# Performance work log

Hardware: AMD Instinct MI355X
Metric: run time of the kernel (lower is better)

## Reference

```python
import jax, jax.numpy as jnp
import numpy as np

B, CIN, COUT, H, W = 16, 128, 128, 64, 64
E, PS, FF = 8, 16, 8
GC, HID, HC = 4 * FF, 64, COUT * 4  # gate_channel, gate hidden, bottleneck hidden


def conv(x, w, stride=1, pad=0, groups=1):
    # x: [B,C,H,W], w: [O,I/groups,kh,kw]
    return jax.lax.conv_general_dilated(
        x, w, (stride, stride), [(pad, pad), (pad, pad)], feature_group_count=groups)


def group_norm(x, scale, bias, groups, eps=1e-5):
    b, c = x.shape[:2]
    xr = x.reshape(b, groups, c // groups, *x.shape[2:])
    m = xr.mean(axis=(2, 3, 4), keepdims=True)
    v = xr.var(axis=(2, 3, 4), keepdims=True)
    xr = (xr - m) * jax.lax.rsqrt(v + eps)
    return xr.reshape(x.shape) * scale[None, :, None, None] + bias[None, :, None, None]


def setup_inputs() -> dict:
    key = jax.random.key(0)
    ks = jax.random.split(key, 8)
    f = lambda k, shp: jax.random.normal(k, shp, jnp.float32) * 0.05
    return dict(
        x=jax.random.normal(ks[0], (B, CIN, H, W), jnp.float32),
        w_exp=f(ks[1], (E, COUT, CIN, 3, 3)),
        gn_exp_s=jnp.ones((E, COUT), jnp.float32),
        gn_exp_b=jnp.zeros((E, COUT), jnp.float32),
        w1=f(ks[2], (GC, HID)), b1=jnp.zeros((HID,), jnp.float32),
        w2=f(ks[3], (HID, E)), b2=jnp.zeros((E,), jnp.float32),
        w_pw1=f(ks[4], (HC, COUT, 1, 1)),
        gn1_s=jnp.ones((HC,), jnp.float32), gn1_b=jnp.zeros((HC,), jnp.float32),
        w_dw=f(ks[5], (HC, 1, 3, 3)),
        gn2_s=jnp.ones((HC,), jnp.float32), gn2_b=jnp.zeros((HC,), jnp.float32),
        w_pw2=f(ks[6], (COUT, HC, 1, 1)),
        gn3_s=jnp.ones((COUT,), jnp.float32), gn3_b=jnp.zeros((COUT,), jnp.float32),
    )


def reference(x, w_exp, gn_exp_s, gn_exp_b, w1, b1, w2, b2,
              w_pw1, gn1_s, gn1_b, w_dw, gn2_s, gn2_b, w_pw2, gn3_s, gn3_b):
    # ---- Conv experts (residual 3x3 conv + GN + SiLU), vmapped over experts ----
    def expert(w, s, b):
        y = conv(x, w, pad=1)
        y = group_norm(y, s, b, groups=min(8, COUT))
        return jax.nn.silu(y) + x  # use_residual=True, CIN == COUT

    ys = jax.vmap(expert)(w_exp, gn_exp_s, gn_exp_b)  # [E,B,C,H,W]

    # ---- Router gate: Fourier features of patch-center coordinates ----
    ph, pw = H // PS, W // PS
    cy = (jnp.arange(ph, dtype=jnp.float32) + 0.5) / ph
    cx = (jnp.arange(pw, dtype=jnp.float32) + 0.5) / pw
    freqs = (2.0 ** jnp.arange(FF, dtype=jnp.float32)) * jnp.pi
    ay = cy[:, None] * freqs  # [ph,FF]
    ax = cx[:, None] * freqs  # [pw,FF]
    feats = jnp.concatenate([
        jnp.broadcast_to(jnp.sin(ay)[:, None, :], (ph, pw, FF)),
        jnp.broadcast_to(jnp.cos(ay)[:, None, :], (ph, pw, FF)),
        jnp.broadcast_to(jnp.sin(ax)[None, :, :], (ph, pw, FF)),
        jnp.broadcast_to(jnp.cos(ax)[None, :, :], (ph, pw, FF)),
    ], axis=-1)  # [ph,pw,4*FF] == gate_channel
    hgate = jax.nn.silu(feats @ w1 + b1)
    wts = jax.nn.softmax(hgate @ w2 + b2, axis=-1)  # [ph,pw,E]

    # ---- Patch-wise combine of expert outputs ----
    wmap = jnp.repeat(jnp.repeat(wts, PS, axis=0), PS, axis=1)  # [H,W,E]
    combined = jnp.einsum('ebchw,hwe->bchw', ys, wmap)

    # ---- Inverted bottleneck: 1x1 -> dw3x3 -> 1x1(stride2) with GN+SiLU ----
    h = jax.nn.silu(group_norm(conv(combined, w_pw1), gn1_s, gn1_b, groups=8))
    h = jax.nn.silu(group_norm(conv(h, w_dw, pad=1, groups=HC), gn2_s, gn2_b, groups=8))
    h = jax.nn.silu(group_norm(conv(h, w_pw2, stride=2), gn3_s, gn3_b, groups=8))
    return h  # [B, COUT, H//2, W//2]
```

## Files before the change

kernel.cpp:

```cpp
#include <hip/hip_runtime.h>
#include <hip/hip_bf16.h>


#define B_ 16
#define CIN_ 128
#define COUT_ 128
#define H_ 64
#define W_ 64
#define HW_ 4096
#define E_ 8
#define FF_ 8
#define GC_ 32
#define HID_ 64
#define HC_ 512

typedef __hip_bfloat16 bf16;
typedef __bf16 bf16x8 __attribute__((ext_vector_type(8)));
typedef float f32x4 __attribute__((ext_vector_type(4)));
typedef float f32x16 __attribute__((ext_vector_type(16)));

__device__ __forceinline__ float siluf(float v) {
  return v * __builtin_amdgcn_rcpf(1.f + __expf(-v));
}
__device__ __forceinline__ float bf2f(bf16 v) { return __bfloat162float(v); }
__device__ __forceinline__ bf16 f2bf(float v) { return __float2bfloat16(v); }

__device__ __forceinline__ void async16(void* lds, const void* g) {
  __builtin_amdgcn_global_load_lds(
      (const __attribute__((address_space(1))) unsigned int*)g,
      (__attribute__((address_space(3))) unsigned int*)lds, 16, 0, 0);
}

__global__ void gate_kernel(const float* __restrict__ w1, const float* __restrict__ b1,
                            const float* __restrict__ w2, const float* __restrict__ b2,
                            float* __restrict__ wts) {
  int p = threadIdx.x;
  if (p >= 16) return;
  int i = p >> 2, j = p & 3;
  float cy = (i + 0.5f) * 0.25f;
  float cx = (j + 0.5f) * 0.25f;
  float feats[GC_];
#pragma unroll
  for (int f = 0; f < FF_; ++f) {
    float fr = 3.14159265358979f * (float)(1 << f);
    float ay = cy * fr, ax = cx * fr;
    feats[f] = sinf(ay);
    feats[FF_ + f] = cosf(ay);
    feats[2 * FF_ + f] = sinf(ax);
    feats[3 * FF_ + f] = cosf(ax);
  }
  float hid[HID_];
  for (int k = 0; k < HID_; ++k) {
    float a = b1[k];
#pragma unroll
    for (int m = 0; m < GC_; ++m) a = fmaf(feats[m], w1[m * HID_ + k], a);
    hid[k] = siluf(a);
  }
  float lg[E_];
  float mx = -1e30f;
#pragma unroll
  for (int e = 0; e < E_; ++e) {
    float a = b2[e];
    for (int k = 0; k < HID_; ++k) a = fmaf(hid[k], w2[k * E_ + e], a);
    lg[e] = a;
    mx = fmaxf(mx, a);
  }
  float s = 0.f;
#pragma unroll
  for (int e = 0; e < E_; ++e) { lg[e] = __expf(lg[e] - mx); s += lg[e]; }
  float inv = 1.f / s;
#pragma unroll
  for (int e = 0; e < E_; ++e) wts[p * E_ + e] = lg[e] * inv;
}

__global__ __launch_bounds__(256) void xt_kernel(const float* __restrict__ x,
                                                 bf16* __restrict__ xT) {
  __shared__ float t[128][65];
  int b = blockIdx.x >> 6, h = blockIdx.x & 63;
  int tid = threadIdx.x;
  int w = tid & 63, c4 = tid >> 6;
  const float* xb = x + ((size_t)(b * 128) * 64 + h) * 64;
#pragma unroll 4
  for (int rep = 0; rep < 32; ++rep) {
    int ci = rep * 4 + c4;
    t[ci][w] = xb[(size_t)ci * HW_ + w];
  }
  __syncthreads();
  bf16* dst = xT + (size_t)(b * 64 + h) * 8192;
#pragma unroll 4
  for (int rep = 0; rep < 32; ++rep) {
    int o = rep * 256 + tid;
    int cg = o >> 9, w2 = (o >> 3) & 63, lo = o & 7;
    dst[o] = f2bf(t[cg * 8 + lo][w2]);
  }
}

__global__ void wt_kernel(const float* __restrict__ w_exp, bf16* __restrict__ wT) {
  int idx = blockIdx.x * 256 + threadIdx.x;
  if (idx >= 1179648) return;
  int lo = idx & 7;
  int co = (idx >> 3) & 127;
  int cg = (idx >> 10) & 15;
  int rest = idx >> 14;
  int tap = rest % 9, e = rest / 9;
  int ci = cg * 8 + lo;
  wT[idx] = f2bf(w_exp[(((size_t)(e * 128 + co) * 128 + ci) * 9) + tap]);
}

__global__ void wpT_kernel(const float* __restrict__ w_pw1, const float* __restrict__ w_pw2,
                           bf16* __restrict__ wp1T, bf16* __restrict__ wp2T) {
  int idx = blockIdx.x * 256 + threadIdx.x;
  if (idx < 65536) wp1T[idx] = f2bf(w_pw1[idx]);
  else if (idx < 131072) wp2T[idx - 65536] = f2bf(w_pw2[idx - 65536]);
}

__global__ __launch_bounds__(256, 2) void conv_mfma(
    const bf16* __restrict__ xT, const bf16* __restrict__ wT,
    float* __restrict__ statsE, bf16* __restrict__ ys) {
  __shared__ __align__(16) char xls[4 * 6336];
  __shared__ __align__(16) char wls[2][3 * 8192];
  __shared__ float red[4][8][2];

  int blk = blockIdx.x;
  int xcd = blk & 7;
  int r2 = blk >> 3;
  int b = xcd * 2 + (r2 & 1);
  int rest = r2 >> 1;
  int rt = rest & 15, e = rest >> 4;

  int tid = threadIdx.x, lane = tid & 63, wave = tid >> 6;
  int hi = lane >> 5, l31 = lane & 31;
  int h0 = rt * 4;

  if (tid < 48) {
    int cg = tid / 12, rem = tid % 12;
    int r = rem >> 1, edge = rem & 1;
    *(uint4*)(xls + cg * 6336 + r * 1056 + edge * 1040) = make_uint4(0u, 0u, 0u, 0u);
  }
  int rbad = (rt == 0) ? 0 : (rt == 15 ? 5 : -1);
  if (rbad >= 0) {
    int cg = tid >> 6, slot = (tid & 63) + 1;
    *(uint4*)(xls + cg * 6336 + rbad * 1056 + slot * 16) = make_uint4(0u, 0u, 0u, 0u);
  }

  f32x16 acc[4][2];
#pragma unroll
  for (int mt = 0; mt < 4; ++mt)
#pragma unroll
    for (int nt = 0; nt < 2; ++nt)
#pragma unroll
      for (int r = 0; r < 16; ++r) acc[mt][nt][r] = 0.f;

  for (int q = 0; q < 4; ++q) {
    if (q) __syncthreads();
    {
      int cg = wave;
#pragma unroll
      for (int r = 0; r < 6; ++r) {
        int h = h0 - 1 + r;
        if ((unsigned)h < 64u) {
          const char* g = (const char*)xT +
              ((size_t)((b * 64 + h) * 16) + q * 4 + cg) * 1024 + lane * 16;
          async16(xls + cg * 6336 + r * 1056 + 16, g);
        }
      }
    }
#pragma unroll
    for (int s = 0; s < 6; ++s) {
      int seg = wave * 6 + s;
      int tap = seg >> 3, rem = seg & 7;
      int cg = rem >> 1, cb = rem & 1;
      const char* g = (const char*)wT +
          ((size_t)(((e * 9 + tap) * 16) + q * 4 + cg) * 128 + cb * 64) * 16 + lane * 16;
      async16(wls[0] + (tap * 4 + cg) * 2048 + cb * 1024, g);
    }
    __syncthreads();

    for (int dr = 0; dr < 3; ++dr) {
      int buf = dr & 1;
      if (dr < 2) {
#pragma unroll
        for (int s = 0; s < 6; ++s) {
          int seg = wave * 6 + s;
          int tap = seg >> 3, rem = seg & 7;
          int cg = rem >> 1, cb = rem & 1;
          const char* g = (const char*)wT +
              ((size_t)(((e * 9 + (dr + 1) * 3 + tap) * 16) + q * 4 + cg) * 128 + cb * 64) * 16 +
              lane * 16;
          async16(wls[buf ^ 1] + (tap * 4 + cg) * 2048 + cb * 1024, g);
        }
      }
      int r_local = wave + dr;
      const char* wb = wls[buf];
      const char* xrow = xls;
      bf16x8 afp[2][2], bfp[2][2];
      {
        int cgl = hi;
        afp[0][0] = *(const bf16x8*)(wb + cgl * 2048 + (0 * 32 + l31) * 16);
        afp[0][1] = *(const bf16x8*)(wb + cgl * 2048 + (1 * 32 + l31) * 16);
        const char* xr = xrow + cgl * 6336 + r_local * 1056;
        bfp[0][0] = *(const bf16x8*)(xr + (0 * 32 + l31 + 0) * 16);
        bfp[0][1] = *(const bf16x8*)(xr + (1 * 32 + l31 + 0) * 16);
      }
#pragma unroll
      for (int s = 0; s < 12; ++s) {
        int mh = s & 1;
        int cura = s & 1, curb = (s >> 1) & 1;
        if (s < 11) {
          int s1 = s + 1;
          int ds1 = s1 >> 2, ks1 = (s1 >> 1) & 1, mh1 = s1 & 1;
          int cgl1 = ks1 * 2 + hi;
          const char* wt1 = wb + ds1 * 8192 + cgl1 * 2048;
          afp[s1 & 1][0] = *(const bf16x8*)(wt1 + ((mh1 * 2 + 0) * 32 + l31) * 16);
          afp[s1 & 1][1] = *(const bf16x8*)(wt1 + ((mh1 * 2 + 1) * 32 + l31) * 16);
          if (mh1 == 0) {
            const char* xr1 = xrow + cgl1 * 6336 + r_local * 1056;
            bfp[(s1 >> 1) & 1][0] = *(const bf16x8*)(xr1 + (0 * 32 + l31 + ds1) * 16);
            bfp[(s1 >> 1) & 1][1] = *(const bf16x8*)(xr1 + (1 * 32 + l31 + ds1) * 16);
          }
        }
#pragma unroll
        for (int i = 0; i < 2; ++i)
#pragma unroll
          for (int nt = 0; nt < 2; ++nt)
            acc[mh * 2 + i][nt] = __builtin_amdgcn_mfma_f32_32x32x16_bf16(
                afp[cura][i], bfp[curb][nt], acc[mh * 2 + i][nt], 0, 0, 0);
      }
      if (dr < 2) __syncthreads();
    }
  }

  int hh = h0 + wave;
  bf16* yb = ys + (size_t)((e * 16 + b) * 128) * 4096;
#pragma unroll
  for (int mt = 0; mt < 4; ++mt) {
    float s0 = 0.f, ss0 = 0.f, s1 = 0.f, ss1 = 0.f;
#pragma unroll
    for (int nt = 0; nt < 2; ++nt) {
      int w = nt * 32 + l31;
      int pos = hh * 64 + w;
#pragma unroll
      for (int r = 0; r < 16; ++r) {
        float v = acc[mt][nt][r];
        if (r < 8) { s0 += v; ss0 += v * v; } else { s1 += v; ss1 += v * v; }
        int row = (r & 3) + 8 * (r >> 2) + 4 * hi;
        yb[(size_t)(mt * 32 + row) * 4096 + pos] = f2bf(v);
      }
    }
#pragma unroll
    for (int off = 32; off; off >>= 1) {
      s0 += __shfl_down(s0, off, 64);
      ss0 += __shfl_down(ss0, off, 64);
      s1 += __shfl_down(s1, off, 64);
      ss1 += __shfl_down(ss1, off, 64);
    }
    if (lane == 0) {
      red[wave][mt * 2][0] = s0; red[wave][mt * 2][1] = ss0;
      red[wave][mt * 2 + 1][0] = s1; red[wave][mt * 2 + 1][1] = ss1;
    }
  }
  __syncthreads();
  if (tid < 16) {
    int g = tid >> 1, which = tid & 1;
    float t = red[0][g][which] + red[1][g][which] + red[2][g][which] + red[3][g][which];
    atomicAdd(&statsE[((e * 16 + b) * 8 + g) * 2 + which], t);
  }
}

__global__ __launch_bounds__(256) void combine_cl(
    const float* __restrict__ x, const bf16* __restrict__ ys,
    const float* __restrict__ stE, const float* __restrict__ gns,
    const float* __restrict__ gnb, const float* __restrict__ wts,
    bf16* __restrict__ ccl) {
  __shared__ bf16 tile[64][132];
  int b = blockIdx.x >> 6, h = blockIdx.x & 63;
  int t = threadIdx.x;
  int oct = t & 7, cq = t >> 3;
  int w0 = oct * 8;
  int gidx = cq >> 2;
  int pid = (h >> 4) * 4 + (w0 >> 4);
  int pos = h * 64 + w0;

  float m_[8], r_[8], wt_[8];
#pragma unroll
  for (int e = 0; e < 8; ++e) {
    float S = stE[((e * 16 + b) * 8 + gidx) * 2];
    float SS = stE[((e * 16 + b) * 8 + gidx) * 2 + 1];
    float mean = S * (1.f / 65536.f);
    float var = SS * (1.f / 65536.f) - mean * mean;
    m_[e] = mean;
    r_[e] = rsqrtf(var + 1e-5f);
    wt_[e] = wts[pid * 8 + e];
  }

#pragma unroll
  for (int k = 0; k < 4; ++k) {
    int co = cq * 4 + k;
    const float* xp = x + ((size_t)(b * 128 + co) << 12) + pos;
    float v[8];
    float4 xa = *(const float4*)xp;
    float4 xb2 = *(const float4*)(xp + 4);
    v[0] = xa.x; v[1] = xa.y; v[2] = xa.z; v[3] = xa.w;
    v[4] = xb2.x; v[5] = xb2.y; v[6] = xb2.z; v[7] = xb2.w;
#pragma unroll
    for (int e = 0; e < 8; ++e) {
      uint4 u = *(const uint4*)(ys + ((size_t)((e * 16 + b) * 128 + co) << 12) + pos);
      const bf16* pv = (const bf16*)&u;
      float sc = r_[e] * gns[e * 128 + co];
      float sh = gnb[e * 128 + co] - m_[e] * sc;
#pragma unroll
      for (int j = 0; j < 8; ++j) {
        float yn = bf2f(pv[j]) * sc + sh;
        v[j] = fmaf(siluf(yn), wt_[e], v[j]);
      }
    }
#pragma unroll
    for (int j = 0; j < 8; ++j) tile[w0 + j][co] = f2bf(v[j]);
  }
  __syncthreads();
  int row = t >> 2, q = t & 3;
  char* dst = (char*)ccl + ((size_t)(b * 4096 + h * 64 + row)) * 256 + q * 64;
  const char* src = (const char*)&tile[row][0] + q * 64;
#pragma unroll
  for (int i = 0; i < 4; ++i)
    *(uint4*)(dst + i * 16) = *(const uint4*)(src + i * 16);
}

__global__ __launch_bounds__(256) void pw1_mfma(
    const bf16* __restrict__ ccl, const bf16* __restrict__ wp1T,
    bf16* __restrict__ h1cl, float* __restrict__ stats1) {
  __shared__ __align__(16) char ls[65536];
  __shared__ float red[4][2][2];
  char* als = ls;
  char* bls = ls + 32768;
  int blk = blockIdx.x;
  int ntile = blk & 511, mtile = blk >> 9;
  int n0 = ntile * 128, m0 = mtile * 128;
  int t = threadIdx.x, lane = t & 63, wave = t >> 6;
  int quad = lane >> 4, l15 = lane & 15;
  int b = n0 >> 12;

#pragma unroll
  for (int i = 0; i < 8; ++i) {
    int id = t + 256 * i;
    int r = id >> 4, c = id & 15;
    *(uint4*)(als + c * 2048 + r * 16) =
        *(const uint4*)((const char*)wp1T + (size_t)(m0 + r) * 256 + c * 16);
    *(uint4*)(bls + c * 2048 + r * 16) =
        *(const uint4*)((const char*)ccl + (size_t)(n0 + r) * 256 + c * 16);
  }
  __syncthreads();

  f32x4 acc[8][2];
#pragma unroll
  for (int mt = 0; mt < 8; ++mt)
#pragma unroll
    for (int nt = 0; nt < 2; ++nt) acc[mt][nt] = (f32x4){0.f, 0.f, 0.f, 0.f};

#pragma unroll
  for (int kc = 0; kc < 4; ++kc) {
    int cgq = kc * 4 + quad;
    bf16x8 af[8];
#pragma unroll
    for (int mt = 0; mt < 8; ++mt)
      af[mt] = *(const bf16x8*)(als + cgq * 2048 + (mt * 16 + l15) * 16);
    bf16x8 bfr[2];
#pragma unroll
    for (int nt = 0; nt < 2; ++nt)
      bfr[nt] = *(const bf16x8*)(bls + cgq * 2048 + (wave * 32 + nt * 16 + l15) * 16);
#pragma unroll
    for (int mt = 0; mt < 8; ++mt)
#pragma unroll
      for (int nt = 0; nt < 2; ++nt)
        acc[mt][nt] = __builtin_amdgcn_mfma_f32_16x16x32_bf16(
            af[mt], bfr[nt], acc[mt][nt], 0, 0, 0);
  }

  __syncthreads();
  float s[2] = {0.f, 0.f}, ss[2] = {0.f, 0.f};
  bf16* tile = (bf16*)ls;
#pragma unroll
  for (int mt = 0; mt < 8; ++mt) {
    int gi = mt >> 2;
#pragma unroll
    for (int nt = 0; nt < 2; ++nt) {
      int n = wave * 32 + nt * 16 + l15;
#pragma unroll
      for (int r = 0; r < 4; ++r) {
        float v = acc[mt][nt][r];
        s[gi] += v;
        ss[gi] += v * v;
        tile[n * 132 + mt * 16 + quad * 4 + r] = f2bf(v);
      }
    }
  }
#pragma unroll
  for (int gi = 0; gi < 2; ++gi) {
#pragma unroll
    for (int off = 32; off; off >>= 1) {
      s[gi] += __shfl_down(s[gi], off, 64);
      ss[gi] += __shfl_down(ss[gi], off, 64);
    }
  }
  if (lane == 0) {
    red[wave][0][0] = s[0]; red[wave][0][1] = ss[0];
    red[wave][1][0] = s[1]; red[wave][1][1] = ss[1];
  }
  __syncthreads();
  if (t < 4) {
    int gi = t >> 1, which = t & 1;
    float v = red[0][gi][which] + red[1][gi][which] + red[2][gi][which] + red[3][gi][which];
    atomicAdd(&stats1[(b * 8 + mtile * 2 + gi) * 2 + which], v);
  }
#pragma unroll
  for (int i = 0; i < 8; ++i) {
    int id = t + 256 * i;
    int r = id >> 4, q = id & 15;
    char* dst = (char*)h1cl + (size_t)(n0 + r) * 1024 + m0 * 2 + q * 16;
    const char* src = (const char*)tile + r * 264 + q * 16;
    *(uint4*)dst = *(const uint4*)src;
  }
}

__global__ __launch_bounds__(256) void dw_cl(
    const bf16* __restrict__ h1cl, const float* __restrict__ w_dw,
    const float* __restrict__ st1, const float* __restrict__ gs,
    const float* __restrict__ gb, bf16* __restrict__ h2cl,
    float* __restrict__ stats2) {
  __shared__ __align__(16) bf16 tile[18 * 66 * 16];
  __shared__ float red2[4][2];
  int blk = blockIdx.x;
  int ht = blk & 3, hcg = (blk >> 2) & 31, b = blk >> 7;
  int h0 = ht * 16;
  int hc0 = hcg * 16;
  int hcb = hcg >> 2;
  int t = threadIdx.x;

  float S1 = st1[(b * 8 + hcb) * 2], SS1 = st1[(b * 8 + hcb) * 2 + 1];
  float mean = S1 * (1.f / 262144.f);
  float var1 = SS1 * (1.f / 262144.f) - mean * mean;
  float rstd = rsqrtf(var1 + 1e-5f);
  float scale[16], shift[16];
#pragma unroll
  for (int j = 0; j < 16; ++j) {
    float g = gs[hc0 + j];
    scale[j] = rstd * g;
    shift[j] = gb[hc0 + j] - mean * rstd * g;
  }

  for (int i = 0; i < 5; ++i) {
    int idx = t + 256 * i;
    if (idx >= 1188) break;
    int row = idx / 66, wslot = idx - row * 66;
    int hh = h0 - 1 + row;
    int w = wslot - 1;
    int swz = (wslot >> 2) & 3;
    bf16* dst = tile + (row * 66 + wslot) * 16;
    if ((unsigned)hh < 64u && (unsigned)w < 64u) {
      const char* p = (const char*)h1cl + ((size_t)(b * 4096 + hh * 64 + w) * 512 + hc0) * 2;
      uint4 a0 = *(const uint4*)p;
      uint4 a1 = *(const uint4*)(p + 16);
      const bf16* pv = (const bf16*)&a0;
      const bf16* pv1 = (const bf16*)&a1;
      bf16 outv[16];
#pragma unroll
      for (int j = 0; j < 8; ++j)
        outv[j] = f2bf(siluf(bf2f(pv[j]) * scale[j] + shift[j]));
#pragma unroll
      for (int j = 0; j < 8; ++j)
        outv[8 + j] = f2bf(siluf(bf2f(pv1[j]) * scale[8 + j] + shift[8 + j]));
#pragma unroll
      for (int qq = 0; qq < 4; ++qq) {
        int ph = (qq + swz) & 3;
        *(uint2*)(dst + ph * 4) = *(const uint2*)(outv + qq * 4);
      }
    } else {
      *(uint4*)dst = make_uint4(0u, 0u, 0u, 0u);
      *(uint4*)(dst + 8) = make_uint4(0u, 0u, 0u, 0u);
    }
  }
  __syncthreads();

  int w = t & 63, q = t >> 6;
  float wv[9][4];
#pragma unroll
  for (int j = 0; j < 4; ++j) {
    int hc = hc0 + q * 4 + j;
#pragma unroll
    for (int tap = 0; tap < 9; ++tap) wv[tap][j] = w_dw[hc * 9 + tap];
  }

  f32x4 win[3][3];
  float acc_s = 0.f, acc_ss = 0.f;

  auto ld4 = [&](int r, int dwi) -> f32x4 {
    int slot = w + dwi;
    int ph = (q + (slot >> 2)) & 3;
    const bf16* p = tile + (r * 66 + slot) * 16 + ph * 4;
    uint2 u = *(const uint2*)p;
    const bf16* pb = (const bf16*)&u;
    return (f32x4){bf2f(pb[0]), bf2f(pb[1]), bf2f(pb[2]), bf2f(pb[3])};
  };

#pragma unroll
  for (int dwi = 0; dwi < 3; ++dwi) {
    win[0][dwi] = ld4(0, dwi);
    win[1][dwi] = ld4(1, dwi);
  }
#pragma unroll
  for (int orow = 0; orow < 16; ++orow) {
    int rnew = orow + 2;
    int ringn = rnew % 3;
#pragma unroll
    for (int dwi = 0; dwi < 3; ++dwi) win[ringn][dwi] = ld4(rnew, dwi);
    f32x4 acc = (f32x4){0.f, 0.f, 0.f, 0.f};
#pragma unroll
    for (int dr = 0; dr < 3; ++dr) {
      int ring = (orow + dr) % 3;
#pragma unroll
      for (int dwi = 0; dwi < 3; ++dwi) {
#pragma unroll
        for (int j = 0; j < 4; ++j)
          acc[j] = fmaf(win[ring][dwi][j], wv[dr * 3 + dwi][j], acc[j]);
      }
    }
#pragma unroll
    for (int j = 0; j < 4; ++j) { acc_s += acc[j]; acc_ss += acc[j] * acc[j]; }
    if (!(orow & 1) && !(w & 1)) {
      int hglob = h0 + orow;
      int pos2 = (hglob >> 1) * 32 + (w >> 1);
      bf16 tmp[4];
#pragma unroll
      for (int j = 0; j < 4; ++j) tmp[j] = f2bf(acc[j]);
      *(uint2*)((char*)h2cl + ((size_t)(b * 1024 + pos2) * 512 + hc0 + q * 4) * 2) =
          *(const uint2*)tmp;
    }
  }

#pragma unroll
  for (int off = 32; off; off >>= 1) {
    acc_s += __shfl_down(acc_s, off, 64);
    acc_ss += __shfl_down(acc_ss, off, 64);
  }
  int wave = t >> 6;
  if ((t & 63) == 0) { red2[wave][0] = acc_s; red2[wave][1] = acc_ss; }
  __syncthreads();
  if (t < 2) {
    float v = red2[0][t] + red2[1][t] + red2[2][t] + red2[3][t];
    atomicAdd(&stats2[(b * 8 + hcb) * 2 + t], v);
  }
}

__global__ __launch_bounds__(256) void pw2_mfma(
    const bf16* __restrict__ h2, const bf16* __restrict__ wp2T,
    const float* __restrict__ st2, const float* __restrict__ gs2,
    const float* __restrict__ gb2, float* __restrict__ h3,
    float* __restrict__ stats3) {
  __shared__ __align__(16) char als[2][8192];
  __shared__ __align__(16) char bls[2][4096];
  __shared__ float red[4][8][2];
  int blk = blockIdx.x;
  int n0 = blk * 64;
  int b = n0 >> 10, posb = n0 & 1023;
  int t = threadIdx.x, lane = t & 63, wave = t >> 6;
  int quad = lane >> 4, l15 = lane & 15;
  int wbase = wave * 16;
  int c4 = t >> 6, r = t & 63;

  auto load_bls = [&](char* dst, int kc) {
    int hc0 = (kc * 4 + c4) * 8;
    int g = hc0 >> 6;
    float S = st2[(b * 8 + g) * 2], SS = st2[(b * 8 + g) * 2 + 1];
    float mean = S * (1.f / 262144.f);
    float rstd = rsqrtf(SS * (1.f / 262144.f) - mean * mean + 1e-5f);
    uint4 u = *(const uint4*)((const char*)h2 + (size_t)(n0 + r) * 1024 +
                              (size_t)(kc * 4 + c4) * 16);
    const bf16* pv = (const bf16*)&u;
    bf16 outv[8];
#pragma unroll
    for (int j = 0; j < 8; ++j) {
      float xv = bf2f(pv[j]);
      xv = (xv - mean) * rstd * gs2[hc0 + j] + gb2[hc0 + j];
      outv[j] = f2bf(siluf(xv));
    }
    *(uint4*)dst = *(const uint4*)outv;
  };

  f32x4 acc[8];
#pragma unroll
  for (int mt = 0; mt < 8; ++mt) acc[mt] = (f32x4){0.f, 0.f, 0.f, 0.f};

  {
#pragma unroll
    for (int i = 0; i < 2; ++i) {
      int id = t + 256 * i;
      int cc = id >> 7, rr = id & 127;
      *(uint4*)(als[0] + cc * 2048 + rr * 16) =
          *(const uint4*)((const char*)wp2T + (size_t)rr * 1024 + cc * 16);
    }
    load_bls(bls[0] + c4 * 1024 + r * 16, 0);
  }
#pragma unroll
  for (int kc = 0; kc < 16; ++kc) {
    __syncthreads();
    if (kc + 1 < 16) {
      int nb = (kc + 1) & 1;
#pragma unroll
      for (int i = 0; i < 2; ++i) {
        int id = t + 256 * i;
        int cc = id >> 7, rr = id & 127;
        *(uint4*)(als[nb] + cc * 2048 + rr * 16) =
            *(const uint4*)((const char*)wp2T + (size_t)rr * 1024 + ((kc + 1) * 4 + cc) * 16);
      }
      load_bls(bls[nb] + c4 * 1024 + r * 16, kc + 1);
    }
    int buf = kc & 1;
    bf16x8 bf1 = *(const bf16x8*)(bls[buf] + quad * 1024 + (wbase + l15) * 16);
#pragma unroll
    for (int mt = 0; mt < 8; ++mt) {
      bf16x8 af = *(const bf16x8*)(als[buf] + quad * 2048 + (mt * 16 + l15) * 16);
      acc[mt] = __builtin_amdgcn_mfma_f32_16x16x32_bf16(af, bf1, acc[mt], 0, 0, 0);
    }
  }

#pragma unroll
  for (int mt = 0; mt < 8; ++mt) {
    float s = 0.f, ss = 0.f;
    int pos = posb + wbase + l15;
#pragma unroll
    for (int rr = 0; rr < 4; ++rr) {
      float v = acc[mt][rr];
      s += v;
      ss += v * v;
      int co = mt * 16 + quad * 4 + rr;
      h3[(size_t)(b * 128 + co) * 1024 + pos] = v;
    }
#pragma unroll
    for (int off = 32; off; off >>= 1) {
      s += __shfl_down(s, off, 64);
      ss += __shfl_down(ss, off, 64);
    }
    if (lane == 0) { red[wave][mt][0] = s; red[wave][mt][1] = ss; }
  }
  __syncthreads();
  if (t < 16) {
    int mt = t >> 1, which = t & 1;
    float v = red[0][mt][which] + red[1][mt][which] + red[2][mt][which] + red[3][mt][which];
    atomicAdd(&stats3[(b * 8 + mt) * 2 + which], v);
  }
}

__global__ void out_kernel(const float* __restrict__ h3, const float* __restrict__ stats,
                           const float* __restrict__ gs, const float* __restrict__ gb,
                           float* __restrict__ out) {
  const int total = B_ * COUT_ * 1024;
  for (int idx = blockIdx.x * blockDim.x + threadIdx.x; idx < total; idx += gridDim.x * blockDim.x) {
    int c = (idx >> 10) & 127;
    int b = idx >> 17;
    int bg = b * 8 + (c >> 4);
    float S = stats[bg * 2], SS = stats[bg * 2 + 1];
    float mean = S * (1.f / 16384.f);
    float var = SS * (1.f / 16384.f) - mean * mean;
    float rstd = rsqrtf(var + 1e-5f);
    float v = (h3[idx] - mean) * rstd * gs[c] + gb[c];
    out[idx] = siluf(v);
  }
}

extern "C" void kernel_launch(void* const* d_in, const int* in_sizes, int n_in,
                              void* d_out, int out_size, void* d_ws, size_t ws_size,
                              hipStream_t stream) {
  const float* x = (const float*)d_in[0];
  const float* w_exp = (const float*)d_in[1];
  const float* gn_exp_s = (const float*)d_in[2];
  const float* gn_exp_b = (const float*)d_in[3];
  const float* w1 = (const float*)d_in[4];
  const float* b1 = (const float*)d_in[5];
  const float* w2 = (const float*)d_in[6];
  const float* b2 = (const float*)d_in[7];
  const float* w_pw1 = (const float*)d_in[8];
  const float* gn1_s = (const float*)d_in[9];
  const float* gn1_b = (const float*)d_in[10];
  const float* w_dw = (const float*)d_in[11];
  const float* gn2_s = (const float*)d_in[12];
  const float* gn2_b = (const float*)d_in[13];
  const float* w_pw2 = (const float*)d_in[14];
  const float* gn3_s = (const float*)d_in[15];
  const float* gn3_b = (const float*)d_in[16];

  char* ws = (char*)d_ws;
  const size_t WP1T_OFF = 16384;
  const size_t WP2T_OFF = WP1T_OFF + 131072;
  const size_t XT_OFF = WP2T_OFF + 131072;
  const size_t WT_OFF = XT_OFF + 16777216;
  const size_t YS_OFF = WT_OFF + 2359296;
  const size_t NEEDED = YS_OFF + 134217728;
  if (ws_size < NEEDED) return;

  float* wts = (float*)ws;
  float* stats1 = (float*)(ws + 1024);
  float* stats2 = (float*)(ws + 2048);
  float* stats3 = (float*)(ws + 3072);
  float* statsE = (float*)(ws + 4096);
  bf16* wp1T = (bf16*)(ws + WP1T_OFF);
  bf16* wp2T = (bf16*)(ws + WP2T_OFF);
  bf16* xT = (bf16*)(ws + XT_OFF);
  bf16* ccl = (bf16*)(ws + XT_OFF);
  bf16* wT = (bf16*)(ws + WT_OFF);
  bf16* ys = (bf16*)(ws + YS_OFF);
  bf16* h1cl = (bf16*)(ws + YS_OFF);
  bf16* h2cl = (bf16*)(ws + YS_OFF + 67108864);
  float* h3 = (float*)(ws + YS_OFF + 83886080);

  hipMemsetAsync(ws, 0, 16384, stream);
  gate_kernel<<<1, 64, 0, stream>>>(w1, b1, w2, b2, wts);
  xt_kernel<<<B_ * 64, 256, 0, stream>>>(x, xT);
  wt_kernel<<<4608, 256, 0, stream>>>(w_exp, wT);
  wpT_kernel<<<512, 256, 0, stream>>>(w_pw1, w_pw2, wp1T, wp2T);
  conv_mfma<<<E_ * B_ * 16, 256, 0, stream>>>(xT, wT, statsE, ys);
  combine_cl<<<B_ * 64, 256, 0, stream>>>(x, ys, statsE, gn_exp_s, gn_exp_b, wts, ccl);
  pw1_mfma<<<4 * 512, 256, 0, stream>>>(ccl, wp1T, h1cl, stats1);
  dw_cl<<<B_ * 32 * 4, 256, 0, stream>>>(h1cl, w_dw, stats1, gn1_s, gn1_b, h2cl, stats2);
  pw2_mfma<<<256, 256, 0, stream>>>(h2cl, wp2T, stats2, gn2_s, gn2_b, h3, stats3);
  out_kernel<<<1024, 256, 0, stream>>>(h3, stats3, gn3_s, gn3_b, (float*)d_out);
}
```

Baseline: 438.6 us.

## Fuse prep kernels, loop pw1 over M tiles, remap combine blocks, vectorize output

Merges the gate, x-transpose, expert-weight and pointwise-weight conversion kernels into one launch, cutting launch overhead. pw1 now loads each activation tile once and loops over the four output-channel tiles instead of launching a block per tile. combine blocks are remapped so a batch stays on one XCD, presumably to reuse ys in that die's cache. The output GN+SiLU kernel processes float4 per thread with a folded scale/shift. The trade-off is fewer blocks in pw1, which lowers parallelism, plus more serialized work per block.

Result: no change. 437.6 us (-0.2%).

```diff
diff --git a/kernel.cpp b/kernel.cpp
--- a/kernel.cpp
+++ b/kernel.cpp
@@ -31,87 +31,89 @@
       (__attribute__((address_space(3))) unsigned int*)lds, 16, 0, 0);
 }
 
-__global__ void gate_kernel(const float* __restrict__ w1, const float* __restrict__ b1,
-                            const float* __restrict__ w2, const float* __restrict__ b2,
-                            float* __restrict__ wts) {
-  int p = threadIdx.x;
-  if (p >= 16) return;
-  int i = p >> 2, j = p & 3;
-  float cy = (i + 0.5f) * 0.25f;
-  float cx = (j + 0.5f) * 0.25f;
-  float feats[GC_];
-#pragma unroll
-  for (int f = 0; f < FF_; ++f) {
-    float fr = 3.14159265358979f * (float)(1 << f);
-    float ay = cy * fr, ax = cx * fr;
-    feats[f] = sinf(ay);
-    feats[FF_ + f] = cosf(ay);
-    feats[2 * FF_ + f] = sinf(ax);
-    feats[3 * FF_ + f] = cosf(ax);
-  }
-  float hid[HID_];
-  for (int k = 0; k < HID_; ++k) {
-    float a = b1[k];
-#pragma unroll
-    for (int m = 0; m < GC_; ++m) a = fmaf(feats[m], w1[m * HID_ + k], a);
-    hid[k] = siluf(a);
-  }
-  float lg[E_];
-  float mx = -1e30f;
-#pragma unroll
-  for (int e = 0; e < E_; ++e) {
-    float a = b2[e];
-    for (int k = 0; k < HID_; ++k) a = fmaf(hid[k], w2[k * E_ + e], a);
-    lg[e] = a;
-    mx = fmaxf(mx, a);
-  }
-  float s = 0.f;
-#pragma unroll
-  for (int e = 0; e < E_; ++e) { lg[e] = __expf(lg[e] - mx); s += lg[e]; }
-  float inv = 1.f / s;
-#pragma unroll
-  for (int e = 0; e < E_; ++e) wts[p * E_ + e] = lg[e] * inv;
-}
-
-__global__ __launch_bounds__(256) void xt_kernel(const float* __restrict__ x,
-                                                 bf16* __restrict__ xT) {
+__global__ __launch_bounds__(256) void prep_kernel(
+    const float* __restrict__ x, bf16* __restrict__ xT,
+    const float* __restrict__ w_exp, bf16* __restrict__ wT,
+    const float* __restrict__ w_pw1, const float* __restrict__ w_pw2,
+    bf16* __restrict__ wp1T, bf16* __restrict__ wp2T,
+    const float* __restrict__ w1, const float* __restrict__ b1,
+    const float* __restrict__ w2, const float* __restrict__ b2,
+    float* __restrict__ wts) {
   __shared__ float t[128][65];
-  int b = blockIdx.x >> 6, h = blockIdx.x & 63;
+  int blk = blockIdx.x;
   int tid = threadIdx.x;
-  int w = tid & 63, c4 = tid >> 6;
-  const float* xb = x + ((size_t)(b * 128) * 64 + h) * 64;
+
+  if (blk < 1024) {
+    int b = blk >> 6, h = blk & 63;
+    int w = tid & 63, c4 = tid >> 6;
+    const float* xb = x + ((size_t)(b * 128) * 64 + h) * 64;
 #pragma unroll 4
-  for (int rep = 0; rep < 32; ++rep) {
-    int ci = rep * 4 + c4;
-    t[ci][w] = xb[(size_t)ci * HW_ + w];
-  }
-  __syncthreads();
-  bf16* dst = xT + (size_t)(b * 64 + h) * 8192;
+    for (int rep = 0; rep < 32; ++rep) {
+      int ci = rep * 4 + c4;
+      t[ci][w] = xb[(size_t)ci * HW_ + w];
+    }
+    __syncthreads();
+    bf16* dst = xT + (size_t)(b * 64 + h) * 8192;
 #pragma unroll 4
-  for (int rep = 0; rep < 32; ++rep) {
-    int o = rep * 256 + tid;
-    int cg = o >> 9, w2 = (o >> 3) & 63, lo = o & 7;
-    dst[o] = f2bf(t[cg * 8 + lo][w2]);
-  }
-}
-
-__global__ void wt_kernel(const float* __restrict__ w_exp, bf16* __restrict__ wT) {
-  int idx = blockIdx.x * 256 + threadIdx.x;
-  if (idx >= 1179648) return;
-  int lo = idx & 7;
-  int co = (idx >> 3) & 127;
-  int cg = (idx >> 10) & 15;
-  int rest = idx >> 14;
-  int tap = rest % 9, e = rest / 9;
-  int ci = cg * 8 + lo;
-  wT[idx] = f2bf(w_exp[(((size_t)(e * 128 + co) * 128 + ci) * 9) + tap]);
-}
-
-__global__ void wpT_kernel(const float* __restrict__ w_pw1, const float* __restrict__ w_pw2,
-                           bf16* __restrict__ wp1T, bf16* __restrict__ wp2T) {
-  int idx = blockIdx.x * 256 + threadIdx.x;
-  if (idx < 65536) wp1T[idx] = f2bf(w_pw1[idx]);
-  else if (idx < 131072) wp2T[idx - 65536] = f2bf(w_pw2[idx - 65536]);
+    for (int rep = 0; rep < 32; ++rep) {
+      int o = rep * 256 + tid;
+      int cg = o >> 9, w2 = (o >> 3) & 63, lo = o & 7;
+      dst[o] = f2bf(t[cg * 8 + lo][w2]);
+    }
+  } else if (blk < 5632) {
+    int idx = (blk - 1024) * 256 + tid;
+    if (idx < 1179648) {
+      int lo = idx & 7;
+      int co = (idx >> 3) & 127;
+      int cg = (idx >> 10) & 15;
+      int rest = idx >> 14;
+      int tap = rest % 9, e = rest / 9;
+      int ci = cg * 8 + lo;
+      wT[idx] = f2bf(w_exp[(((size_t)(e * 128 + co) * 128 + ci) * 9) + tap]);
+    }
+  } else if (blk < 6144) {
+    int idx = (blk - 5632) * 256 + tid;
+    if (idx < 65536) wp1T[idx] = f2bf(w_pw1[idx]);
+    else wp2T[idx - 65536] = f2bf(w_pw2[idx - 65536]);
+  } else {
+    int p = tid;
+    if (p >= 16) return;
+    int i = p >> 2, j = p & 3;
+    float cy = (i + 0.5f) * 0.25f;
+    float cx = (j + 0.5f) * 0.25f;
+    float feats[GC_];
+#pragma unroll
+    for (int f = 0; f < FF_; ++f) {
+      float fr = 3.14159265358979f * (float)(1 << f);
+      float ay = cy * fr, ax = cx * fr;
+      feats[f] = sinf(ay);
+      feats[FF_ + f] = cosf(ay);
+      feats[2 * FF_ + f] = sinf(ax);
+      feats[3 * FF_ + f] = cosf(ax);
+    }
+    float hid[HID_];
+    for (int k = 0; k < HID_; ++k) {
+      float a = b1[k];
+#pragma unroll
+      for (int m = 0; m < GC_; ++m) a = fmaf(feats[m], w1[m * HID_ + k], a);
+      hid[k] = siluf(a);
+    }
+    float lg[E_];
+    float mx = -1e30f;
+#pragma unroll
+    for (int e = 0; e < E_; ++e) {
+      float a = b2[e];
+      for (int k = 0; k < HID_; ++k) a = fmaf(hid[k], w2[k * E_ + e], a);
+      lg[e] = a;
+      mx = fmaxf(mx, a);
+    }
+    float s = 0.f;
+#pragma unroll
+    for (int e = 0; e < E_; ++e) { lg[e] = __expf(lg[e] - mx); s += lg[e]; }
+    float inv = 1.f / s;
+#pragma unroll
+    for (int e = 0; e < E_; ++e) wts[p * E_ + e] = lg[e] * inv;
+  }
 }
 
 __global__ __launch_bounds__(256, 2) void conv_mfma(
@@ -273,7 +275,11 @@
     const float* __restrict__ gnb, const float* __restrict__ wts,
     bf16* __restrict__ ccl) {
   __shared__ bf16 tile[64][132];
-  int b = blockIdx.x >> 6, h = blockIdx.x & 63;
+  int blk = blockIdx.x;
+  int xcd = blk & 7;
+  int k2 = blk >> 3;
+  int b = xcd * 2 + (k2 >> 6);
+  int h = k2 & 63;
   int t = threadIdx.x;
   int oct = t & 7, cq = t >> 3;
   int w0 = oct * 8;
@@ -329,13 +335,11 @@
 __global__ __launch_bounds__(256) void pw1_mfma(
     const bf16* __restrict__ ccl, const bf16* __restrict__ wp1T,
     bf16* __restrict__ h1cl, float* __restrict__ stats1) {
-  __shared__ __align__(16) char ls[65536];
+  __shared__ __align__(16) char bls[32768];
+  __shared__ __align__(16) char ls2[34816];
   __shared__ float red[4][2][2];
-  char* als = ls;
-  char* bls = ls + 32768;
   int blk = blockIdx.x;
-  int ntile = blk & 511, mtile = blk >> 9;
-  int n0 = ntile * 128, m0 = mtile * 128;
+  int n0 = blk * 128;
   int t = threadIdx.x, lane = t & 63, wave = t >> 6;
   int quad = lane >> 4, l15 = lane & 15;
   int b = n0 >> 12;
@@ -344,81 +348,92 @@
   for (int i = 0; i < 8; ++i) {
     int id = t + 256 * i;
     int r = id >> 4, c = id & 15;
-    *(uint4*)(als + c * 2048 + r * 16) =
-        *(const uint4*)((const char*)wp1T + (size_t)(m0 + r) * 256 + c * 16);
     *(uint4*)(bls + c * 2048 + r * 16) =
         *(const uint4*)((const char*)ccl + (size_t)(n0 + r) * 256 + c * 16);
   }
-  __syncthreads();
-
-  f32x4 acc[8][2];
-#pragma unroll
-  for (int mt = 0; mt < 8; ++mt)
-#pragma unroll
-    for (int nt = 0; nt < 2; ++nt) acc[mt][nt] = (f32x4){0.f, 0.f, 0.f, 0.f};
-
-#pragma unroll
-  for (int kc = 0; kc < 4; ++kc) {
-    int cgq = kc * 4 + quad;
-    bf16x8 af[8];
+
+  for (int mtile = 0; mtile < 4; ++mtile) {
+    int m0 = mtile * 128;
+    char* als = ls2;
+#pragma unroll
+    for (int i = 0; i < 8; ++i) {
+      int id = t + 256 * i;
+      int r = id >> 4, c = id & 15;
+      *(uint4*)(als + c * 2048 + r * 16) =
+          *(const uint4*)((const char*)wp1T + (size_t)(m0 + r) * 256 + c * 16);
+    }
+    __syncthreads();
+
+    f32x4 acc[8][2];
 #pragma unroll
     for (int mt = 0; mt < 8; ++mt)
-      af[mt] = *(const bf16x8*)(als + cgq * 2048 + (mt * 16 + l15) * 16);
-    bf16x8 bfr[2];
-#pragma unroll
-    for (int nt = 0; nt < 2; ++nt)
-      bfr[nt] = *(const bf16x8*)(bls + cgq * 2048 + (wave * 32 + nt * 16 + l15) * 16);
-#pragma unroll
-    for (int mt = 0; mt < 8; ++mt)
+#pragma unroll
+      for (int nt = 0; nt < 2; ++nt) acc[mt][nt] = (f32x4){0.f, 0.f, 0.f, 0.f};
+
+#pragma unroll
+    for (int kc = 0; kc < 4; ++kc) {
+      int cgq = kc * 4 + quad;
+      bf16x8 af[8];
+#pragma unroll
+      for (int mt = 0; mt < 8; ++mt)
+        af[mt] = *(const bf16x8*)(als + cgq * 2048 + (mt * 16 + l15) * 16);
+      bf16x8 bfr[2];
 #pragma unroll
       for (int nt = 0; nt < 2; ++nt)
-        acc[mt][nt] = __builtin_amdgcn_mfma_f32_16x16x32_bf16(
-            af[mt], bfr[nt], acc[mt][nt], 0, 0, 0);
-  }
-
-  __syncthreads();
-  float s[2] = {0.f, 0.f}, ss[2] = {0.f, 0.f};
-  bf16* tile = (bf16*)ls;
-#pragma unroll
-  for (int mt = 0; mt < 8; ++mt) {
-    int gi = mt >> 2;
-#pragma unroll
-    for (int nt = 0; nt < 2; ++nt) {
-      int n = wave * 32 + nt * 16 + l15;
-#pragma unroll
-      for (int r = 0; r < 4; ++r) {
-        float v = acc[mt][nt][r];
-        s[gi] += v;
-        ss[gi] += v * v;
-        tile[n * 132 + mt * 16 + quad * 4 + r] = f2bf(v);
-      }
-    }
-  }
-#pragma unroll
-  for (int gi = 0; gi < 2; ++gi) {
-#pragma unroll
-    for (int off = 32; off; off >>= 1) {
-      s[gi] += __shfl_down(s[gi], off, 64);
-      ss[gi] += __shfl_down(ss[gi], off, 64);
-    }
-  }
-  if (lane == 0) {
-    red[wave][0][0] = s[0]; red[wave][0][1] = ss[0];
-    red[wave][1][0] = s[1]; red[wave][1][1] = ss[1];
-  }
-  __syncthreads();
-  if (t < 4) {
-    int gi = t >> 1, which = t & 1;
-    float v = red[0][gi][which] + red[1][gi][which] + red[2][gi][which] + red[3][gi][which];
-    atomicAdd(&stats1[(b * 8 + mtile * 2 + gi) * 2 + which], v);
-  }
-#pragma unroll
-  for (int i = 0; i < 8; ++i) {
-    int id = t + 256 * i;
-    int r = id >> 4, q = id & 15;
-    char* dst = (char*)h1cl + (size_t)(n0 + r) * 1024 + m0 * 2 + q * 16;
-    const char* src = (const char*)tile + r * 264 + q * 16;
-    *(uint4*)dst = *(const uint4*)src;
+        bfr[nt] = *(const bf16x8*)(bls + cgq * 2048 + (wave * 32 + nt * 16 + l15) * 16);
+#pragma unroll
+      for (int mt = 0; mt < 8; ++mt)
+#pragma unroll
+        for (int nt = 0; nt < 2; ++nt)
+          acc[mt][nt] = __builtin_amdgcn_mfma_f32_16x16x32_bf16(
+              af[mt], bfr[nt], acc[mt][nt], 0, 0, 0);
+    }
+
+    __syncthreads();
+    float s[2] = {0.f, 0.f}, ss[2] = {0.f, 0.f};
+    bf16* tile = (bf16*)ls2;
+#pragma unroll
+    for (int mt = 0; mt < 8; ++mt) {
+      int gi = mt >> 2;
+#pragma unroll
+      for (int nt = 0; nt < 2; ++nt) {
+        int n = wave * 32 + nt * 16 + l15;
+#pragma unroll
+        for (int r = 0; r < 4; ++r) {
+          float v = acc[mt][nt][r];
+          s[gi] += v;
+          ss[gi] += v * v;
+          tile[n * 132 + mt * 16 + quad * 4 + r] = f2bf(v);
+        }
+      }
+    }
+#pragma unroll
+    for (int gi = 0; gi < 2; ++gi) {
+#pragma unroll
+      for (int off = 32; off; off >>= 1) {
+        s[gi] += __shfl_down(s[gi], off, 64);
+        ss[gi] += __shfl_down(ss[gi], off, 64);
+      }
+    }
+    if (lane == 0) {
+      red[wave][0][0] = s[0]; red[wave][0][1] = ss[0];
+      red[wave][1][0] = s[1]; red[wave][1][1] = ss[1];
+    }
+    __syncthreads();
+    if (t < 4) {
+      int gi = t >> 1, which = t & 1;
+      float v = red[0][gi][which] + red[1][gi][which] + red[2][gi][which] + red[3][gi][which];
+      atomicAdd(&stats1[(b * 8 + mtile * 2 + gi) * 2 + which], v);
+    }
+#pragma unroll
+    for (int i = 0; i < 8; ++i) {
+      int id = t + 256 * i;
+      int r = id >> 4, q = id & 15;
+      char* dst = (char*)h1cl + (size_t)(n0 + r) * 1024 + m0 * 2 + q * 16;
+      const char* src = (const char*)tile + r * 264 + q * 16;
+      *(uint4*)dst = *(const uint4*)src;
+    }
+    __syncthreads();
   }
 }
 
@@ -653,8 +668,10 @@
 __global__ void out_kernel(const float* __restrict__ h3, const float* __restrict__ stats,
                            const float* __restrict__ gs, const float* __restrict__ gb,
                            float* __restrict__ out) {
-  const int total = B_ * COUT_ * 1024;
-  for (int idx = blockIdx.x * blockDim.x + threadIdx.x; idx < total; idx += gridDim.x * blockDim.x) {
+  const int total4 = (B_ * COUT_ * 1024) >> 2;
+  for (int i4 = blockIdx.x * blockDim.x + threadIdx.x; i4 < total4;
+       i4 += gridDim.x * blockDim.x) {
+    int idx = i4 << 2;
     int c = (idx >> 10) & 127;
     int b = idx >> 17;
     int bg = b * 8 + (c >> 4);
@@ -662,8 +679,15 @@
     float mean = S * (1.f / 16384.f);
     float var = SS * (1.f / 16384.f) - mean * mean;
     float rstd = rsqrtf(var + 1e-5f);
-    float v = (h3[idx] - mean) * rstd * gs[c] + gb[c];
-    out[idx] = siluf(v);
+    float sc = rstd * gs[c];
+    float sh = gb[c] - mean * sc;
+    float4 hv = *(const float4*)(h3 + idx);
+    float4 res;
+    res.x = siluf(hv.x * sc + sh);
+    res.y = siluf(hv.y * sc + sh);
+    res.z = siluf(hv.z * sc + sh);
+    res.w = siluf(hv.w * sc + sh);
+    *(float4*)(out + idx) = res;
   }
 }
 
@@ -713,13 +737,11 @@
   float* h3 = (float*)(ws + YS_OFF + 83886080);
 
   hipMemsetAsync(ws, 0, 16384, stream);
-  gate_kernel<<<1, 64, 0, stream>>>(w1, b1, w2, b2, wts);
-  xt_kernel<<<B_ * 64, 256, 0, stream>>>(x, xT);
-  wt_kernel<<<4608, 256, 0, stream>>>(w_exp, wT);
-  wpT_kernel<<<512, 256, 0, stream>>>(w_pw1, w_pw2, wp1T, wp2T);
+  prep_kernel<<<6145, 256, 0, stream>>>(x, xT, w_exp, wT, w_pw1, w_pw2, wp1T, wp2T,
+                                        w1, b1, w2, b2, wts);
   conv_mfma<<<E_ * B_ * 16, 256, 0, stream>>>(xT, wT, statsE, ys);
   combine_cl<<<B_ * 64, 256, 0, stream>>>(x, ys, statsE, gn_exp_s, gn_exp_b, wts, ccl);
-  pw1_mfma<<<4 * 512, 256, 0, stream>>>(ccl, wp1T, h1cl, stats1);
+  pw1_mfma<<<512, 256, 0, stream>>>(ccl, wp1T, h1cl, stats1);
   dw_cl<<<B_ * 32 * 4, 256, 0, stream>>>(h1cl, w_dw, stats1, gn1_s, gn1_b, h2cl, stats2);
   pw2_mfma<<<256, 256, 0, stream>>>(h2cl, wp2T, stats2, gn2_s, gn2_b, h3, stats3);
   out_kernel<<<1024, 256, 0, stream>>>(h3, stats3, gn3_s, gn3_b, (float*)d_out);
```
